# Kernel tuning notes

Hardware: AMD Instinct MI355X
Metric: run time of the kernel (lower is better)

Reference implementation:

```python
import jax, jax.numpy as jnp
import numpy as np

N_NODES = 50000
N_EDGES = 800000
F_IN = 64
HID = 64
N_GRAPHS = 256
BN_EPS = 1e-5


def setup_inputs() -> dict:
    key = jax.random.key(0)
    ks = jax.random.split(key, 16)
    inp = {
        'x': jax.random.normal(ks[0], (N_NODES, F_IN), dtype=jnp.float32),
        'edge_index': jax.random.randint(ks[1], (2, N_EDGES), 0, N_NODES, dtype=jnp.int64),
        'edge_weight': jax.random.uniform(ks[2], (N_EDGES,), dtype=jnp.float32),
        'batch': jnp.sort(jax.random.randint(ks[3], (N_NODES,), 0, N_GRAPHS, dtype=jnp.int64)),
    }
    def lin(k, fi, fo):
        s = 1.0 / np.sqrt(fi)
        kw, kb = jax.random.split(k)
        return (jax.random.uniform(kw, (fi, fo), jnp.float32, -s, s),
                jax.random.uniform(kb, (fo,), jnp.float32, -s, s))
    inp['W1'], inp['b1'] = lin(ks[4], F_IN, HID)
    inp['W2'], inp['b2'] = lin(ks[5], HID, HID)
    inp['W3'], inp['b3'] = lin(ks[6], HID, HID)
    inp['fcW1'], inp['fcb1'] = lin(ks[7], HID, HID)
    inp['fcW2'], inp['fcb2'] = lin(ks[8], HID, 1)
    for i, k in zip((1, 2, 3), ks[9:12]):
        inp[f'g{i}'] = jnp.ones((HID,), jnp.float32)
        inp[f'be{i}'] = jnp.zeros((HID,), jnp.float32)
    return inp


def gin_conv(x, src, dst, edge_weight, W, b):
    # weighted scatter-add aggregation: agg[dst] += w_e * x[src]
    msg = x[src] * edge_weight[:, None]            # [E, d]
    agg = jax.ops.segment_sum(msg, dst, num_segments=x.shape[0])  # [N, d]
    return (x + agg) @ W + b                       # GIN eps=0, nn = Linear


def batch_norm(x, gamma, beta):
    mu = jnp.mean(x, axis=0)
    var = jnp.var(x, axis=0)
    return (x - mu) * jax.lax.rsqrt(var + BN_EPS) * gamma + beta


def reference(x, edge_index, edge_weight, batch,
              W1, b1, W2, b2, W3, b3, fcW1, fcb1, fcW2, fcb2,
              g1, be1, g2, be2, g3, be3):
    src, dst = edge_index[0], edge_index[1]
    h = batch_norm(jax.nn.relu(gin_conv(x, src, dst, edge_weight, W1, b1)), g1, be1)
    h = batch_norm(jax.nn.relu(gin_conv(h, src, dst, edge_weight, W2, b2)), g2, be2)
    h = batch_norm(gin_conv(h, src, dst, edge_weight, W3, b3), g3, be3)
    pooled = jax.ops.segment_sum(h, batch, num_segments=N_GRAPHS)  # global_add_pool
    h = jax.nn.relu(pooled)
    h = jax.nn.relu(h @ fcW1 + fcb1)
    # dropout is identity in eval / deterministic reference
    return (h @ fcW2 + fcb2).reshape(-1)
```

## Files before the change

### kernel.cpp

```cpp
#include <hip/hip_runtime.h>
#include <hip/hip_bf16.h>


#define NN 50000
#define NE 800000
#define FD 64
#define NG 256
#define CAP 64
#define BN_EPS 1e-5f


__global__ __launch_bounds__(256) void build_slots_kernel(
    const int* __restrict__ src, const int* __restrict__ dst,
    const float* __restrict__ ew, int* __restrict__ cursor,
    uint2* __restrict__ slots)
{
    int e = blockIdx.x * 256 + threadIdx.x;
    if (e < NE) {
        int d = dst[e];
        int pos = atomicAdd(&cursor[d], 1) & (CAP - 1);
        slots[(size_t)d * CAP + pos] = make_uint2((unsigned)src[e],
                                                  __float_as_uint(ew[e]));
    }
}

__global__ __launch_bounds__(256) void agg_layer_kernel(
    const float* __restrict__ h, const int* __restrict__ deg,
    const uint2* __restrict__ slots, const float* __restrict__ affine,
    const float* __restrict__ W, const float* __restrict__ b,
    float* __restrict__ y, float* __restrict__ buckets, int relu_flag)
{
    __shared__ float Ws[FD * FD];
    __shared__ float ps1[4][FD];
    __shared__ float ps2[4][FD];
    int tid  = threadIdx.x;
    int wave = tid >> 6, lane = tid & 63;
    int g = lane >> 4, l = lane & 15;
    int node = blockIdx.x * 4 + wave;

    {
        float4* Wv = (float4*)Ws;
        const float4* Wg = (const float4*)W;
        #pragma unroll
        for (int i = 0; i < 4; i++) Wv[tid + 256 * i] = Wg[tid + 256 * i];
    }

    const float4* __restrict__ h4 = (const float4*)h;

    uint2 ms = slots[(size_t)node * CAP + lane];
    int dg = deg[node];
    float4 self = h4[(size_t)node * 16 + l];
    if (dg > CAP) dg = CAP;

    __syncthreads();

    float4 acc = make_float4(0.f, 0.f, 0.f, 0.f);
    float wsum = 0.f;
    int nIter = (dg + 7) >> 3;
    for (int i = 0; i < nIter; i++) {
        int e0 = 8 * i + g;
        int e1 = e0 + 4;
        int ee0 = (e0 < dg) ? e0 : 0;
        int ee1 = (e1 < dg) ? e1 : 0;
        int   s0 = __shfl((int)ms.x, ee0, 64);
        int   s1 = __shfl((int)ms.x, ee1, 64);
        float w0 = __uint_as_float((unsigned)__shfl((int)ms.y, ee0, 64));
        float w1 = __uint_as_float((unsigned)__shfl((int)ms.y, ee1, 64));
        w0 = (e0 < dg) ? w0 : 0.f;
        w1 = (e1 < dg) ? w1 : 0.f;
        float4 v0 = h4[(size_t)s0 * 16 + l];
        float4 v1 = h4[(size_t)s1 * 16 + l];
        wsum += w0 + w1;
        acc.x = fmaf(w0, v0.x, acc.x); acc.y = fmaf(w0, v0.y, acc.y);
        acc.z = fmaf(w0, v0.z, acc.z); acc.w = fmaf(w0, v0.w, acc.w);
        acc.x = fmaf(w1, v1.x, acc.x); acc.y = fmaf(w1, v1.y, acc.y);
        acc.z = fmaf(w1, v1.z, acc.z); acc.w = fmaf(w1, v1.w, acc.w);
    }
    acc.x += __shfl_xor(acc.x, 16, 64); acc.y += __shfl_xor(acc.y, 16, 64);
    acc.z += __shfl_xor(acc.z, 16, 64); acc.w += __shfl_xor(acc.w, 16, 64);
    wsum  += __shfl_xor(wsum, 16, 64);
    acc.x += __shfl_xor(acc.x, 32, 64); acc.y += __shfl_xor(acc.y, 32, 64);
    acc.z += __shfl_xor(acc.z, 32, 64); acc.w += __shfl_xor(acc.w, 32, 64);
    wsum  += __shfl_xor(wsum, 32, 64);

    float4 raw;
    raw.x = self.x + acc.x; raw.y = self.y + acc.y;
    raw.z = self.z + acc.z; raw.w = self.w + acc.w;

    float4 af = make_float4(1.f, 1.f, 1.f, 1.f);
    float4 cf = make_float4(0.f, 0.f, 0.f, 0.f);
    if (affine) {
        af = ((const float4*)affine)[l];
        cf = ((const float4*)(affine + FD))[l];
    }
    float sw = 1.0f + wsum;
    float4 hin;
    hin.x = fmaf(af.x, raw.x, cf.x * sw);
    hin.y = fmaf(af.y, raw.y, cf.y * sw);
    hin.z = fmaf(af.z, raw.z, cf.z * sw);
    hin.w = fmaf(af.w, raw.w, cf.w * sw);

    const float4* __restrict__ WsV = (const float4*)Ws;
    float4 yp = make_float4(0.f, 0.f, 0.f, 0.f);
    #pragma unroll
    for (int kk = 0; kk < 4; kk++) {
        int srcl = 4 * g + kk;
        float a0 = __shfl(hin.x, srcl, 64);
        float a1 = __shfl(hin.y, srcl, 64);
        float a2 = __shfl(hin.z, srcl, 64);
        float a3 = __shfl(hin.w, srcl, 64);
        int k0 = 16 * g + 4 * kk;
        float4 w0 = WsV[(k0 + 0) * 16 + l];
        float4 w1 = WsV[(k0 + 1) * 16 + l];
        float4 w2 = WsV[(k0 + 2) * 16 + l];
        float4 w3 = WsV[(k0 + 3) * 16 + l];
        yp.x = fmaf(a0, w0.x, yp.x); yp.y = fmaf(a0, w0.y, yp.y);
        yp.z = fmaf(a0, w0.z, yp.z); yp.w = fmaf(a0, w0.w, yp.w);
        yp.x = fmaf(a1, w1.x, yp.x); yp.y = fmaf(a1, w1.y, yp.y);
        yp.z = fmaf(a1, w1.z, yp.z); yp.w = fmaf(a1, w1.w, yp.w);
        yp.x = fmaf(a2, w2.x, yp.x); yp.y = fmaf(a2, w2.y, yp.y);
        yp.z = fmaf(a2, w2.z, yp.z); yp.w = fmaf(a2, w2.w, yp.w);
        yp.x = fmaf(a3, w3.x, yp.x); yp.y = fmaf(a3, w3.y, yp.y);
        yp.z = fmaf(a3, w3.z, yp.z); yp.w = fmaf(a3, w3.w, yp.w);
    }
    yp.x += __shfl_xor(yp.x, 16, 64); yp.y += __shfl_xor(yp.y, 16, 64);
    yp.z += __shfl_xor(yp.z, 16, 64); yp.w += __shfl_xor(yp.w, 16, 64);
    yp.x += __shfl_xor(yp.x, 32, 64); yp.y += __shfl_xor(yp.y, 32, 64);
    yp.z += __shfl_xor(yp.z, 32, 64); yp.w += __shfl_xor(yp.w, 32, 64);

    float4 bias = ((const float4*)b)[l];
    float4 yv;
    yv.x = yp.x + bias.x; yv.y = yp.y + bias.y;
    yv.z = yp.z + bias.z; yv.w = yp.w + bias.w;
    if (relu_flag) {
        yv.x = fmaxf(yv.x, 0.f); yv.y = fmaxf(yv.y, 0.f);
        yv.z = fmaxf(yv.z, 0.f); yv.w = fmaxf(yv.w, 0.f);
    }
    if (g == 0) {
        ((float4*)y)[(size_t)node * 16 + l] = yv;
        ((float4*)&ps1[wave][0])[l] = yv;
        float4 sq;
        sq.x = yv.x * yv.x; sq.y = yv.y * yv.y;
        sq.z = yv.z * yv.z; sq.w = yv.w * yv.w;
        ((float4*)&ps2[wave][0])[l] = sq;
    }
    __syncthreads();
    if (tid < FD) {
        float a = ps1[0][tid] + ps1[1][tid] + ps1[2][tid] + ps1[3][tid];
        float q = ps2[0][tid] + ps2[1][tid] + ps2[2][tid] + ps2[3][tid];
        float* bk = buckets + (blockIdx.x & 63) * 128;
        atomicAdd(&bk[tid], a);
        atomicAdd(&bk[FD + tid], q);
    }
}

__global__ __launch_bounds__(256) void finalize_kernel(
    const float* __restrict__ buckets, const float* __restrict__ gamma,
    const float* __restrict__ beta, float* __restrict__ affine)
{
    __shared__ float part[4][2][FD];
    int tid = threadIdx.x;
    int f = tid & 63, q = tid >> 6;
    float S1 = 0.f, S2 = 0.f;
    #pragma unroll
    for (int i = 0; i < 16; i++) {
        int bkt = q * 16 + i;
        S1 += buckets[bkt * 128 + f];
        S2 += buckets[bkt * 128 + FD + f];
    }
    part[q][0][f] = S1;
    part[q][1][f] = S2;
    __syncthreads();
    if (tid < FD) {
        float s1 = part[0][0][tid] + part[1][0][tid] + part[2][0][tid] + part[3][0][tid];
        float s2 = part[0][1][tid] + part[1][1][tid] + part[2][1][tid] + part[3][1][tid];
        float mu  = s1 * (1.f / NN);
        float var = s2 * (1.f / NN) - mu * mu;
        float af = gamma[tid] * rsqrtf(var + BN_EPS);
        affine[tid]      = af;
        affine[FD + tid] = beta[tid] - mu * af;
    }
}

__global__ __launch_bounds__(256) void pool_head_kernel(
    const float* __restrict__ y, const int* __restrict__ batch,
    const float* __restrict__ affine3,
    const float* __restrict__ fcW1, const float* __restrict__ fcb1,
    const float* __restrict__ fcW2, const float* __restrict__ fcb2,
    float* __restrict__ out)
{
    __shared__ float red[16][FD];
    __shared__ int bounds[2];
    int tid = threadIdx.x;
    int g = blockIdx.x;
    if (tid < 2) {
        int target = g + tid;
        int lo = 0, hi = NN;
        while (lo < hi) {
            int mid = (lo + hi) >> 1;
            if (batch[mid] < target) lo = mid + 1; else hi = mid;
        }
        bounds[tid] = lo;
    }
    __syncthreads();
    int s = bounds[0], e = bounds[1];
    int l = tid & 15, r = tid >> 4;
    const float4* __restrict__ y4 = (const float4*)y;
    float4 acc = make_float4(0.f, 0.f, 0.f, 0.f);
    for (int n = s + r; n < e; n += 16) {
        float4 v = y4[(size_t)n * 16 + l];
        acc.x += v.x; acc.y += v.y; acc.z += v.z; acc.w += v.w;
    }
    ((float4*)&red[r][0])[l] = acc;
    __syncthreads();
    for (int off = 8; off > 0; off >>= 1) {
        if (r < off) {
            float4 a = ((float4*)&red[r][0])[l];
            float4 o = ((float4*)&red[r + off][0])[l];
            a.x += o.x; a.y += o.y; a.z += o.z; a.w += o.w;
            ((float4*)&red[r][0])[l] = a;
        }
        __syncthreads();
    }
    if (tid < 64) {
        float cnt = (float)(e - s);
        float p = red[0][tid];
        p = fmaf(affine3[tid], p, affine3[FD + tid] * cnt);
        p = fmaxf(p, 0.f);
        float acc1 = fcb1[tid];
        #pragma unroll
        for (int k = 0; k < FD; k++) {
            float pk = __shfl(p, k, 64);
            acc1 = fmaf(pk, fcW1[k * FD + tid], acc1);
        }
        acc1 = fmaxf(acc1, 0.f);
        float prod = acc1 * fcW2[tid];
        #pragma unroll
        for (int off = 32; off > 0; off >>= 1)
            prod += __shfl_xor(prod, off, 64);
        if (tid == 0) out[g] = prod + fcb2[0];
    }
}

extern "C" void kernel_launch(void* const* d_in, const int* in_sizes, int n_in,
                              void* d_out, int out_size, void* d_ws, size_t ws_size,
                              hipStream_t stream) {
    const float* x     = (const float*)d_in[0];
    const int*   ei    = (const int*)d_in[1];
    const float* ew    = (const float*)d_in[2];
    const int*   batch = (const int*)d_in[3];
    const float* W1 = (const float*)d_in[4],  *b1 = (const float*)d_in[5];
    const float* W2 = (const float*)d_in[6],  *b2 = (const float*)d_in[7];
    const float* W3 = (const float*)d_in[8],  *b3 = (const float*)d_in[9];
    const float* fcW1 = (const float*)d_in[10], *fcb1 = (const float*)d_in[11];
    const float* fcW2 = (const float*)d_in[12], *fcb2 = (const float*)d_in[13];
    const float* g1 = (const float*)d_in[14], *be1 = (const float*)d_in[15];
    const float* g2 = (const float*)d_in[16], *be2 = (const float*)d_in[17];
    const float* g3 = (const float*)d_in[18], *be3 = (const float*)d_in[19];
    float* out = (float*)d_out;

    const int* srcp = ei;
    const int* dstp = ei + NE;

    char* ws = (char*)d_ws;
    size_t off = 0;
    auto take = [&](size_t bytes) -> char* {
        char* p = ws + off;
        off += (bytes + 255) & ~(size_t)255;
        return p;
    };
    float* bufA    = (float*)take((size_t)NN * FD * 4);
    float* bufB    = (float*)take((size_t)NN * FD * 4);
    uint2* slots   = (uint2*)take((size_t)NN * CAP * 8);
    float* affine  = (float*)take((size_t)3 * 2 * FD * 4);
    size_t zero_base = off;
    int*   cursor  = (int*)  take((size_t)NN * 4);
    float* buckets = (float*)take((size_t)3 * 64 * 128 * 4);
    size_t zero_bytes = off - zero_base;
    (void)ws_size; (void)n_in; (void)in_sizes; (void)out_size;

    hipMemsetAsync(ws + zero_base, 0, zero_bytes, stream);

    build_slots_kernel<<<(NE + 255) / 256, 256, 0, stream>>>(srcp, dstp, ew,
                                                             cursor, slots);

    const int gridA = NN / 4;

    float* bk1 = buckets + 0 * 64 * 128;
    float* bk2 = buckets + 1 * 64 * 128;
    float* bk3 = buckets + 2 * 64 * 128;
    float* af1 = affine + 0 * 128;
    float* af2 = affine + 1 * 128;
    float* af3 = affine + 2 * 128;

    agg_layer_kernel<<<gridA, 256, 0, stream>>>(x, cursor, slots,
                                                nullptr, W1, b1, bufA, bk1, 1);
    finalize_kernel<<<1, 256, 0, stream>>>(bk1, g1, be1, af1);
    agg_layer_kernel<<<gridA, 256, 0, stream>>>(bufA, cursor, slots,
                                                af1, W2, b2, bufB, bk2, 1);
    finalize_kernel<<<1, 256, 0, stream>>>(bk2, g2, be2, af2);
    agg_layer_kernel<<<gridA, 256, 0, stream>>>(bufB, cursor, slots,
                                                af2, W3, b3, bufA, bk3, 0);
    finalize_kernel<<<1, 256, 0, stream>>>(bk3, g3, be3, af3);
    pool_head_kernel<<<NG, 256, 0, stream>>>(bufA, batch, af3,
                                             fcW1, fcb1, fcW2, fcb2, out);
}
```

Before: 292.0 us.

## Process four nodes per wave and replace atomic BN buckets with per-block partials

Each agg_layer block now handles 16 nodes (4 per wave, strided across the grid), so the 16KB weight tile load into shared memory is amortised over four times as many nodes, and slot/degree loads for all four nodes are issued up front. BN statistics are accumulated in registers across the four nodes and written as per-block partials instead of atomically added to 64 buckets. A new 64-block reduce-and-finalize kernel sums the 3125 partials per feature. The trade-off is fewer blocks, less parallelism and a serial loop over four nodes per wave, plus an extra partial buffer to read.

New measurement: 326.5 us. +11.8%, slower.

```diff
diff --git a/kernel.cpp b/kernel.cpp
--- a/kernel.cpp
+++ b/kernel.cpp
@@ -7,6 +7,7 @@
 #define FD 64
 #define NG 256
 #define CAP 64
+#define NBLK 3125
 #define BN_EPS 1e-5f
 
 
@@ -28,7 +29,7 @@
     const float* __restrict__ h, const int* __restrict__ deg,
     const uint2* __restrict__ slots, const float* __restrict__ affine,
     const float* __restrict__ W, const float* __restrict__ b,
-    float* __restrict__ y, float* __restrict__ buckets, int relu_flag)
+    float* __restrict__ y, float* __restrict__ partial, int relu_flag)
 {
     __shared__ float Ws[FD * FD];
     __shared__ float ps1[4][FD];
@@ -36,7 +37,6 @@
     int tid  = threadIdx.x;
     int wave = tid >> 6, lane = tid & 63;
     int g = lane >> 4, l = lane & 15;
-    int node = blockIdx.x * 4 + wave;
 
     {
         float4* Wv = (float4*)Ws;
@@ -47,45 +47,16 @@
 
     const float4* __restrict__ h4 = (const float4*)h;
 
-    uint2 ms = slots[(size_t)node * CAP + lane];
-    int dg = deg[node];
-    float4 self = h4[(size_t)node * 16 + l];
-    if (dg > CAP) dg = CAP;
-
-    __syncthreads();
-
-    float4 acc = make_float4(0.f, 0.f, 0.f, 0.f);
-    float wsum = 0.f;
-    int nIter = (dg + 7) >> 3;
-    for (int i = 0; i < nIter; i++) {
-        int e0 = 8 * i + g;
-        int e1 = e0 + 4;
-        int ee0 = (e0 < dg) ? e0 : 0;
-        int ee1 = (e1 < dg) ? e1 : 0;
-        int   s0 = __shfl((int)ms.x, ee0, 64);
-        int   s1 = __shfl((int)ms.x, ee1, 64);
-        float w0 = __uint_as_float((unsigned)__shfl((int)ms.y, ee0, 64));
-        float w1 = __uint_as_float((unsigned)__shfl((int)ms.y, ee1, 64));
-        w0 = (e0 < dg) ? w0 : 0.f;
-        w1 = (e1 < dg) ? w1 : 0.f;
-        float4 v0 = h4[(size_t)s0 * 16 + l];
-        float4 v1 = h4[(size_t)s1 * 16 + l];
-        wsum += w0 + w1;
-        acc.x = fmaf(w0, v0.x, acc.x); acc.y = fmaf(w0, v0.y, acc.y);
-        acc.z = fmaf(w0, v0.z, acc.z); acc.w = fmaf(w0, v0.w, acc.w);
-        acc.x = fmaf(w1, v1.x, acc.x); acc.y = fmaf(w1, v1.y, acc.y);
-        acc.z = fmaf(w1, v1.z, acc.z); acc.w = fmaf(w1, v1.w, acc.w);
-    }
-    acc.x += __shfl_xor(acc.x, 16, 64); acc.y += __shfl_xor(acc.y, 16, 64);
-    acc.z += __shfl_xor(acc.z, 16, 64); acc.w += __shfl_xor(acc.w, 16, 64);
-    wsum  += __shfl_xor(wsum, 16, 64);
-    acc.x += __shfl_xor(acc.x, 32, 64); acc.y += __shfl_xor(acc.y, 32, 64);
-    acc.z += __shfl_xor(acc.z, 32, 64); acc.w += __shfl_xor(acc.w, 32, 64);
-    wsum  += __shfl_xor(wsum, 32, 64);
-
-    float4 raw;
-    raw.x = self.x + acc.x; raw.y = self.y + acc.y;
-    raw.z = self.z + acc.z; raw.w = self.w + acc.w;
+    int nodes[4], dgs[4];
+    uint2 mss[4];
+    #pragma unroll
+    for (int k = 0; k < 4; k++) {
+        nodes[k] = (k * NBLK + blockIdx.x) * 4 + wave;
+        dgs[k] = deg[nodes[k]];
+    }
+    #pragma unroll
+    for (int k = 0; k < 4; k++)
+        mss[k] = slots[(size_t)nodes[k] * CAP + lane];
 
     float4 af = make_float4(1.f, 1.f, 1.f, 1.f);
     float4 cf = make_float4(0.f, 0.f, 0.f, 0.f);
@@ -93,92 +64,140 @@
         af = ((const float4*)affine)[l];
         cf = ((const float4*)(affine + FD))[l];
     }
-    float sw = 1.0f + wsum;
-    float4 hin;
-    hin.x = fmaf(af.x, raw.x, cf.x * sw);
-    hin.y = fmaf(af.y, raw.y, cf.y * sw);
-    hin.z = fmaf(af.z, raw.z, cf.z * sw);
-    hin.w = fmaf(af.w, raw.w, cf.w * sw);
+    float4 bias = ((const float4*)b)[l];
+
+    __syncthreads();
 
     const float4* __restrict__ WsV = (const float4*)Ws;
-    float4 yp = make_float4(0.f, 0.f, 0.f, 0.f);
+    float4 s1 = make_float4(0.f, 0.f, 0.f, 0.f);
+    float4 s2 = make_float4(0.f, 0.f, 0.f, 0.f);
+
     #pragma unroll
-    for (int kk = 0; kk < 4; kk++) {
-        int srcl = 4 * g + kk;
-        float a0 = __shfl(hin.x, srcl, 64);
-        float a1 = __shfl(hin.y, srcl, 64);
-        float a2 = __shfl(hin.z, srcl, 64);
-        float a3 = __shfl(hin.w, srcl, 64);
-        int k0 = 16 * g + 4 * kk;
-        float4 w0 = WsV[(k0 + 0) * 16 + l];
-        float4 w1 = WsV[(k0 + 1) * 16 + l];
-        float4 w2 = WsV[(k0 + 2) * 16 + l];
-        float4 w3 = WsV[(k0 + 3) * 16 + l];
-        yp.x = fmaf(a0, w0.x, yp.x); yp.y = fmaf(a0, w0.y, yp.y);
-        yp.z = fmaf(a0, w0.z, yp.z); yp.w = fmaf(a0, w0.w, yp.w);
-        yp.x = fmaf(a1, w1.x, yp.x); yp.y = fmaf(a1, w1.y, yp.y);
-        yp.z = fmaf(a1, w1.z, yp.z); yp.w = fmaf(a1, w1.w, yp.w);
-        yp.x = fmaf(a2, w2.x, yp.x); yp.y = fmaf(a2, w2.y, yp.y);
-        yp.z = fmaf(a2, w2.z, yp.z); yp.w = fmaf(a2, w2.w, yp.w);
-        yp.x = fmaf(a3, w3.x, yp.x); yp.y = fmaf(a3, w3.y, yp.y);
-        yp.z = fmaf(a3, w3.z, yp.z); yp.w = fmaf(a3, w3.w, yp.w);
-    }
-    yp.x += __shfl_xor(yp.x, 16, 64); yp.y += __shfl_xor(yp.y, 16, 64);
-    yp.z += __shfl_xor(yp.z, 16, 64); yp.w += __shfl_xor(yp.w, 16, 64);
-    yp.x += __shfl_xor(yp.x, 32, 64); yp.y += __shfl_xor(yp.y, 32, 64);
-    yp.z += __shfl_xor(yp.z, 32, 64); yp.w += __shfl_xor(yp.w, 32, 64);
-
-    float4 bias = ((const float4*)b)[l];
-    float4 yv;
-    yv.x = yp.x + bias.x; yv.y = yp.y + bias.y;
-    yv.z = yp.z + bias.z; yv.w = yp.w + bias.w;
-    if (relu_flag) {
-        yv.x = fmaxf(yv.x, 0.f); yv.y = fmaxf(yv.y, 0.f);
-        yv.z = fmaxf(yv.z, 0.f); yv.w = fmaxf(yv.w, 0.f);
-    }
+    for (int k = 0; k < 4; k++) {
+        int node = nodes[k];
+        int dg = dgs[k] > CAP ? CAP : dgs[k];
+        uint2 ms = mss[k];
+        float4 self = h4[(size_t)node * 16 + l];
+
+        float4 acc = make_float4(0.f, 0.f, 0.f, 0.f);
+        float wsum = 0.f;
+        int nIter = (dg + 7) >> 3;
+        for (int i = 0; i < nIter; i++) {
+            int e0 = 8 * i + g;
+            int e1 = e0 + 4;
+            int ee0 = (e0 < dg) ? e0 : 0;
+            int ee1 = (e1 < dg) ? e1 : 0;
+            int   sA = __shfl((int)ms.x, ee0, 64);
+            int   sB = __shfl((int)ms.x, ee1, 64);
+            float w0 = __uint_as_float((unsigned)__shfl((int)ms.y, ee0, 64));
+            float w1 = __uint_as_float((unsigned)__shfl((int)ms.y, ee1, 64));
+            w0 = (e0 < dg) ? w0 : 0.f;
+            w1 = (e1 < dg) ? w1 : 0.f;
+            float4 v0 = h4[(size_t)sA * 16 + l];
+            float4 v1 = h4[(size_t)sB * 16 + l];
+            wsum += w0 + w1;
+            acc.x = fmaf(w0, v0.x, acc.x); acc.y = fmaf(w0, v0.y, acc.y);
+            acc.z = fmaf(w0, v0.z, acc.z); acc.w = fmaf(w0, v0.w, acc.w);
+            acc.x = fmaf(w1, v1.x, acc.x); acc.y = fmaf(w1, v1.y, acc.y);
+            acc.z = fmaf(w1, v1.z, acc.z); acc.w = fmaf(w1, v1.w, acc.w);
+        }
+        acc.x += __shfl_xor(acc.x, 16, 64); acc.y += __shfl_xor(acc.y, 16, 64);
+        acc.z += __shfl_xor(acc.z, 16, 64); acc.w += __shfl_xor(acc.w, 16, 64);
+        wsum  += __shfl_xor(wsum, 16, 64);
+        acc.x += __shfl_xor(acc.x, 32, 64); acc.y += __shfl_xor(acc.y, 32, 64);
+        acc.z += __shfl_xor(acc.z, 32, 64); acc.w += __shfl_xor(acc.w, 32, 64);
+        wsum  += __shfl_xor(wsum, 32, 64);
+
+        float4 raw;
+        raw.x = self.x + acc.x; raw.y = self.y + acc.y;
+        raw.z = self.z + acc.z; raw.w = self.w + acc.w;
+
+        float sw = 1.0f + wsum;
+        float4 hin;
+        hin.x = fmaf(af.x, raw.x, cf.x * sw);
+        hin.y = fmaf(af.y, raw.y, cf.y * sw);
+        hin.z = fmaf(af.z, raw.z, cf.z * sw);
+        hin.w = fmaf(af.w, raw.w, cf.w * sw);
+
+        float4 yp = make_float4(0.f, 0.f, 0.f, 0.f);
+        #pragma unroll
+        for (int kk = 0; kk < 4; kk++) {
+            int srcl = 4 * g + kk;
+            float a0 = __shfl(hin.x, srcl, 64);
+            float a1 = __shfl(hin.y, srcl, 64);
+            float a2 = __shfl(hin.z, srcl, 64);
+            float a3 = __shfl(hin.w, srcl, 64);
+            int k0 = 16 * g + 4 * kk;
+            float4 w0 = WsV[(k0 + 0) * 16 + l];
+            float4 w1 = WsV[(k0 + 1) * 16 + l];
+            float4 w2 = WsV[(k0 + 2) * 16 + l];
+            float4 w3 = WsV[(k0 + 3) * 16 + l];
+            yp.x = fmaf(a0, w0.x, yp.x); yp.y = fmaf(a0, w0.y, yp.y);
+            yp.z = fmaf(a0, w0.z, yp.z); yp.w = fmaf(a0, w0.w, yp.w);
+            yp.x = fmaf(a1, w1.x, yp.x); yp.y = fmaf(a1, w1.y, yp.y);
+            yp.z = fmaf(a1, w1.z, yp.z); yp.w = fmaf(a1, w1.w, yp.w);
+            yp.x = fmaf(a2, w2.x, yp.x); yp.y = fmaf(a2, w2.y, yp.y);
+            yp.z = fmaf(a2, w2.z, yp.z); yp.w = fmaf(a2, w2.w, yp.w);
+            yp.x = fmaf(a3, w3.x, yp.x); yp.y = fmaf(a3, w3.y, yp.y);
+            yp.z = fmaf(a3, w3.z, yp.z); yp.w = fmaf(a3, w3.w, yp.w);
+        }
+        yp.x += __shfl_xor(yp.x, 16, 64); yp.y += __shfl_xor(yp.y, 16, 64);
+        yp.z += __shfl_xor(yp.z, 16, 64); yp.w += __shfl_xor(yp.w, 16, 64);
+        yp.x += __shfl_xor(yp.x, 32, 64); yp.y += __shfl_xor(yp.y, 32, 64);
+        yp.z += __shfl_xor(yp.z, 32, 64); yp.w += __shfl_xor(yp.w, 32, 64);
+
+        float4 yv;
+        yv.x = yp.x + bias.x; yv.y = yp.y + bias.y;
+        yv.z = yp.z + bias.z; yv.w = yp.w + bias.w;
+        if (relu_flag) {
+            yv.x = fmaxf(yv.x, 0.f); yv.y = fmaxf(yv.y, 0.f);
+            yv.z = fmaxf(yv.z, 0.f); yv.w = fmaxf(yv.w, 0.f);
+        }
+        if (g == 0)
+            ((float4*)y)[(size_t)node * 16 + l] = yv;
+        s1.x += yv.x; s1.y += yv.y; s1.z += yv.z; s1.w += yv.w;
+        s2.x = fmaf(yv.x, yv.x, s2.x); s2.y = fmaf(yv.y, yv.y, s2.y);
+        s2.z = fmaf(yv.z, yv.z, s2.z); s2.w = fmaf(yv.w, yv.w, s2.w);
+    }
+
     if (g == 0) {
-        ((float4*)y)[(size_t)node * 16 + l] = yv;
-        ((float4*)&ps1[wave][0])[l] = yv;
-        float4 sq;
-        sq.x = yv.x * yv.x; sq.y = yv.y * yv.y;
-        sq.z = yv.z * yv.z; sq.w = yv.w * yv.w;
-        ((float4*)&ps2[wave][0])[l] = sq;
+        ((float4*)&ps1[wave][0])[l] = s1;
+        ((float4*)&ps2[wave][0])[l] = s2;
     }
     __syncthreads();
     if (tid < FD) {
         float a = ps1[0][tid] + ps1[1][tid] + ps1[2][tid] + ps1[3][tid];
         float q = ps2[0][tid] + ps2[1][tid] + ps2[2][tid] + ps2[3][tid];
-        float* bk = buckets + (blockIdx.x & 63) * 128;
-        atomicAdd(&bk[tid], a);
-        atomicAdd(&bk[FD + tid], q);
-    }
-}
-
-__global__ __launch_bounds__(256) void finalize_kernel(
-    const float* __restrict__ buckets, const float* __restrict__ gamma,
+        partial[(size_t)blockIdx.x * 128 + tid]      = a;
+        partial[(size_t)blockIdx.x * 128 + 64 + tid] = q;
+    }
+}
+
+__global__ __launch_bounds__(256) void redfin_kernel(
+    const float* __restrict__ partial, const float* __restrict__ gamma,
     const float* __restrict__ beta, float* __restrict__ affine)
 {
-    __shared__ float part[4][2][FD];
+    __shared__ float red[256];
     int tid = threadIdx.x;
-    int f = tid & 63, q = tid >> 6;
-    float S1 = 0.f, S2 = 0.f;
-    #pragma unroll
-    for (int i = 0; i < 16; i++) {
-        int bkt = q * 16 + i;
-        S1 += buckets[bkt * 128 + f];
-        S2 += buckets[bkt * 128 + FD + f];
-    }
-    part[q][0][f] = S1;
-    part[q][1][f] = S2;
-    __syncthreads();
-    if (tid < FD) {
-        float s1 = part[0][0][tid] + part[1][0][tid] + part[2][0][tid] + part[3][0][tid];
-        float s2 = part[0][1][tid] + part[1][1][tid] + part[2][1][tid] + part[3][1][tid];
-        float mu  = s1 * (1.f / NN);
-        float var = s2 * (1.f / NN) - mu * mu;
-        float af = gamma[tid] * rsqrtf(var + BN_EPS);
-        affine[tid]      = af;
-        affine[FD + tid] = beta[tid] - mu * af;
+    int B = blockIdx.x;
+    int half = tid >> 7;
+    int t = tid & 127;
+    int f = B + half * 64;
+    float s = 0.f;
+    for (int j = t; j < NBLK; j += 128) s += partial[(size_t)j * 128 + f];
+    red[tid] = s;
+    __syncthreads();
+    for (int off = 64; off >= 1; off >>= 1) {
+        if ((tid & 127) < off) red[tid] += red[tid + off];
+        __syncthreads();
+    }
+    if (tid == 0) {
+        float S1 = red[0], S2 = red[128];
+        float mu  = S1 * (1.f / NN);
+        float var = S2 * (1.f / NN) - mu * mu;
+        float a = gamma[B] * rsqrtf(var + BN_EPS);
+        affine[B]      = a;
+        affine[FD + B] = beta[B] - mu * a;
     }
 }
 
@@ -273,9 +292,9 @@
     float* bufB    = (float*)take((size_t)NN * FD * 4);
     uint2* slots   = (uint2*)take((size_t)NN * CAP * 8);
     float* affine  = (float*)take((size_t)3 * 2 * FD * 4);
+    float* partial = (float*)take((size_t)NBLK * 128 * 4);
     size_t zero_base = off;
     int*   cursor  = (int*)  take((size_t)NN * 4);
-    float* buckets = (float*)take((size_t)3 * 64 * 128 * 4);
     size_t zero_bytes = off - zero_base;
     (void)ws_size; (void)n_in; (void)in_sizes; (void)out_size;
 
@@ -284,24 +303,19 @@
     build_slots_kernel<<<(NE + 255) / 256, 256, 0, stream>>>(srcp, dstp, ew,
                                                              cursor, slots);
 
-    const int gridA = NN / 4;
-
-    float* bk1 = buckets + 0 * 64 * 128;
-    float* bk2 = buckets + 1 * 64 * 128;
-    float* bk3 = buckets + 2 * 64 * 128;
     float* af1 = affine + 0 * 128;
     float* af2 = affine + 1 * 128;
     float* af3 = affine + 2 * 128;
 
-    agg_layer_kernel<<<gridA, 256, 0, stream>>>(x, cursor, slots,
-                                                nullptr, W1, b1, bufA, bk1, 1);
-    finalize_kernel<<<1, 256, 0, stream>>>(bk1, g1, be1, af1);
-    agg_layer_kernel<<<gridA, 256, 0, stream>>>(bufA, cursor, slots,
-                                                af1, W2, b2, bufB, bk2, 1);
-    finalize_kernel<<<1, 256, 0, stream>>>(bk2, g2, be2, af2);
-    agg_layer_kernel<<<gridA, 256, 0, stream>>>(bufB, cursor, slots,
-                                                af2, W3, b3, bufA, bk3, 0);
-    finalize_kernel<<<1, 256, 0, stream>>>(bk3, g3, be3, af3);
+    agg_layer_kernel<<<NBLK, 256, 0, stream>>>(x, cursor, slots,
+                                               nullptr, W1, b1, bufA, partial, 1);
+    redfin_kernel<<<64, 256, 0, stream>>>(partial, g1, be1, af1);
+    agg_layer_kernel<<<NBLK, 256, 0, stream>>>(bufA, cursor, slots,
+                                               af1, W2, b2, bufB, partial, 1);
+    redfin_kernel<<<64, 256, 0, stream>>>(partial, g2, be2, af2);
+    agg_layer_kernel<<<NBLK, 256, 0, stream>>>(bufB, cursor, slots,
+                                               af2, W3, b3, bufA, partial, 0);
+    redfin_kernel<<<64, 256, 0, stream>>>(partial, g3, be3, af3);
     pool_head_kernel<<<NG, 256, 0, stream>>>(bufA, batch, af3,
                                              fcW1, fcb1, fcW2, fcb2, out);
 }
```

## Store node features in bf16 and pack edge slots into 32 bits

Applied to the files above, without the earlier changes.

Node feature buffers are now kept in bf16, halving the bytes moved in the random gather over neighbours and in the pool reads. Input x is converted once by a new kernel. Edge slots pack a 16-bit source index with a bf16 weight into one 32-bit word, halving slot traffic. The cost is reduced precision in features and edge weights. The 16-bit source field cannot hold node indices of 65536 or more; this holds for 50000 nodes but ties the code to that size.

After: 287.8 us. Within noise of the previous version (-1.4%).

```diff
diff --git a/kernel.cpp b/kernel.cpp
--- a/kernel.cpp
+++ b/kernel.cpp
@@ -9,26 +9,51 @@
 #define CAP 64
 #define BN_EPS 1e-5f
 
+__device__ __forceinline__ float4 dec4(uint2 a) {
+    float4 f;
+    f.x = __uint_as_float(a.x << 16);
+    f.y = __uint_as_float(a.x & 0xFFFF0000u);
+    f.z = __uint_as_float(a.y << 16);
+    f.w = __uint_as_float(a.y & 0xFFFF0000u);
+    return f;
+}
+__device__ __forceinline__ unsigned rbf(float f) {
+    unsigned u = __float_as_uint(f);
+    return (u + 0x7FFFu + ((u >> 16) & 1u)) >> 16;
+}
+__device__ __forceinline__ uint2 enc4(float4 v) {
+    uint2 o;
+    o.x = rbf(v.x) | (rbf(v.y) << 16);
+    o.y = rbf(v.z) | (rbf(v.w) << 16);
+    return o;
+}
 
 __global__ __launch_bounds__(256) void build_slots_kernel(
     const int* __restrict__ src, const int* __restrict__ dst,
     const float* __restrict__ ew, int* __restrict__ cursor,
-    uint2* __restrict__ slots)
+    unsigned* __restrict__ slots)
 {
     int e = blockIdx.x * 256 + threadIdx.x;
     if (e < NE) {
         int d = dst[e];
         int pos = atomicAdd(&cursor[d], 1) & (CAP - 1);
-        slots[(size_t)d * CAP + pos] = make_uint2((unsigned)src[e],
-                                                  __float_as_uint(ew[e]));
-    }
+        slots[(size_t)d * CAP + pos] =
+            ((unsigned)src[e] << 16) | rbf(ew[e]);
+    }
+}
+
+__global__ __launch_bounds__(256) void cvt_kernel(
+    const float4* __restrict__ xin, uint2* __restrict__ xout)
+{
+    int i = blockIdx.x * 256 + threadIdx.x;
+    xout[i] = enc4(xin[i]);
 }
 
 __global__ __launch_bounds__(256) void agg_layer_kernel(
-    const float* __restrict__ h, const int* __restrict__ deg,
-    const uint2* __restrict__ slots, const float* __restrict__ affine,
+    const uint2* __restrict__ h, const int* __restrict__ deg,
+    const unsigned* __restrict__ slots, const float* __restrict__ affine,
     const float* __restrict__ W, const float* __restrict__ b,
-    float* __restrict__ y, float* __restrict__ buckets, int relu_flag)
+    uint2* __restrict__ y, float* __restrict__ buckets, int relu_flag)
 {
     __shared__ float Ws[FD * FD];
     __shared__ float ps1[4][FD];
@@ -45,11 +70,9 @@
         for (int i = 0; i < 4; i++) Wv[tid + 256 * i] = Wg[tid + 256 * i];
     }
 
-    const float4* __restrict__ h4 = (const float4*)h;
-
-    uint2 ms = slots[(size_t)node * CAP + lane];
+    unsigned ms = slots[(size_t)node * CAP + lane];
     int dg = deg[node];
-    float4 self = h4[(size_t)node * 16 + l];
+    float4 self = dec4(h[(size_t)node * 16 + l]);
     if (dg > CAP) dg = CAP;
 
     __syncthreads();
@@ -62,14 +85,14 @@
         int e1 = e0 + 4;
         int ee0 = (e0 < dg) ? e0 : 0;
         int ee1 = (e1 < dg) ? e1 : 0;
-        int   s0 = __shfl((int)ms.x, ee0, 64);
-        int   s1 = __shfl((int)ms.x, ee1, 64);
-        float w0 = __uint_as_float((unsigned)__shfl((int)ms.y, ee0, 64));
-        float w1 = __uint_as_float((unsigned)__shfl((int)ms.y, ee1, 64));
+        unsigned m0 = (unsigned)__shfl((int)ms, ee0, 64);
+        unsigned m1 = (unsigned)__shfl((int)ms, ee1, 64);
+        float w0 = __uint_as_float((m0 & 0xFFFFu) << 16);
+        float w1 = __uint_as_float((m1 & 0xFFFFu) << 16);
         w0 = (e0 < dg) ? w0 : 0.f;
         w1 = (e1 < dg) ? w1 : 0.f;
-        float4 v0 = h4[(size_t)s0 * 16 + l];
-        float4 v1 = h4[(size_t)s1 * 16 + l];
+        float4 v0 = dec4(h[(size_t)(m0 >> 16) * 16 + l]);
+        float4 v1 = dec4(h[(size_t)(m1 >> 16) * 16 + l]);
         wsum += w0 + w1;
         acc.x = fmaf(w0, v0.x, acc.x); acc.y = fmaf(w0, v0.y, acc.y);
         acc.z = fmaf(w0, v0.z, acc.z); acc.w = fmaf(w0, v0.w, acc.w);
@@ -137,7 +160,7 @@
         yv.z = fmaxf(yv.z, 0.f); yv.w = fmaxf(yv.w, 0.f);
     }
     if (g == 0) {
-        ((float4*)y)[(size_t)node * 16 + l] = yv;
+        y[(size_t)node * 16 + l] = enc4(yv);
         ((float4*)&ps1[wave][0])[l] = yv;
         float4 sq;
         sq.x = yv.x * yv.x; sq.y = yv.y * yv.y;
@@ -176,14 +199,14 @@
         float s2 = part[0][1][tid] + part[1][1][tid] + part[2][1][tid] + part[3][1][tid];
         float mu  = s1 * (1.f / NN);
         float var = s2 * (1.f / NN) - mu * mu;
-        float af = gamma[tid] * rsqrtf(var + BN_EPS);
-        affine[tid]      = af;
-        affine[FD + tid] = beta[tid] - mu * af;
+        float a = gamma[tid] * rsqrtf(var + BN_EPS);
+        affine[tid]      = a;
+        affine[FD + tid] = beta[tid] - mu * a;
     }
 }
 
 __global__ __launch_bounds__(256) void pool_head_kernel(
-    const float* __restrict__ y, const int* __restrict__ batch,
+    const uint2* __restrict__ y, const int* __restrict__ batch,
     const float* __restrict__ affine3,
     const float* __restrict__ fcW1, const float* __restrict__ fcb1,
     const float* __restrict__ fcW2, const float* __restrict__ fcb2,
@@ -205,10 +228,9 @@
     __syncthreads();
     int s = bounds[0], e = bounds[1];
     int l = tid & 15, r = tid >> 4;
-    const float4* __restrict__ y4 = (const float4*)y;
     float4 acc = make_float4(0.f, 0.f, 0.f, 0.f);
     for (int n = s + r; n < e; n += 16) {
-        float4 v = y4[(size_t)n * 16 + l];
+        float4 v = dec4(y[(size_t)n * 16 + l]);
         acc.x += v.x; acc.y += v.y; acc.z += v.z; acc.w += v.w;
     }
     ((float4*)&red[r][0])[l] = acc;
@@ -269,13 +291,14 @@
         off += (bytes + 255) & ~(size_t)255;
         return p;
     };
-    float* bufA    = (float*)take((size_t)NN * FD * 4);
-    float* bufB    = (float*)take((size_t)NN * FD * 4);
-    uint2* slots   = (uint2*)take((size_t)NN * CAP * 8);
-    float* affine  = (float*)take((size_t)3 * 2 * FD * 4);
+    uint2*    xbf   = (uint2*)   take((size_t)NN * FD * 2);
+    uint2*    bufA  = (uint2*)   take((size_t)NN * FD * 2);
+    uint2*    bufB  = (uint2*)   take((size_t)NN * FD * 2);
+    unsigned* slots = (unsigned*)take((size_t)NN * CAP * 4);
+    float*    affine= (float*)   take((size_t)3 * 2 * FD * 4);
     size_t zero_base = off;
-    int*   cursor  = (int*)  take((size_t)NN * 4);
-    float* buckets = (float*)take((size_t)3 * 64 * 128 * 4);
+    int*      cursor= (int*)     take((size_t)NN * 4);
+    float*    buckets=(float*)   take((size_t)3 * 64 * 128 * 4);
     size_t zero_bytes = off - zero_base;
     (void)ws_size; (void)n_in; (void)in_sizes; (void)out_size;
 
@@ -283,6 +306,7 @@
 
     build_slots_kernel<<<(NE + 255) / 256, 256, 0, stream>>>(srcp, dstp, ew,
                                                              cursor, slots);
+    cvt_kernel<<<(NN * 16) / 256, 256, 0, stream>>>((const float4*)x, xbf);
 
     const int gridA = NN / 4;
 
@@ -293,7 +317,7 @@
     float* af2 = affine + 1 * 128;
     float* af3 = affine + 2 * 128;
 
-    agg_layer_kernel<<<gridA, 256, 0, stream>>>(x, cursor, slots,
+    agg_layer_kernel<<<gridA, 256, 0, stream>>>(xbf, cursor, slots,
                                                 nullptr, W1, b1, bufA, bk1, 1);
     finalize_kernel<<<1, 256, 0, stream>>>(bk1, g1, be1, af1);
     agg_layer_kernel<<<gridA, 256, 0, stream>>>(bufA, cursor, slots,
```
